# Kernel optimization log

Hardware: AMD Instinct MI355X
Metric: run time of the kernel (lower is better)

Reference implementation:

```python
import jax, jax.numpy as jnp
import numpy as np

N_NODES = 100000
N_EDGES = 3200000
F_IN = 512
F_OUT = 256


def setup_inputs() -> dict:
    key = jax.random.key(0)
    k1, k2, k3, k4, k5 = jax.random.split(key, 5)
    x = jax.random.normal(k1, (N_NODES, F_IN), dtype=jnp.float32)
    weights = jax.random.normal(k2, (F_IN, F_OUT), dtype=jnp.float32) * 0.05
    # sparse adjacency in COO, row-sorted (equivalent to the CSR torch.spmm uses)
    edge_row = jnp.sort(jax.random.randint(k3, (N_EDGES,), 0, N_NODES, dtype=jnp.int32))
    edge_col = jax.random.randint(k4, (N_EDGES,), 0, N_NODES, dtype=jnp.int32)
    edge_val = jax.random.uniform(k5, (N_EDGES,), dtype=jnp.float32)
    return {"x": x, "weights": weights, "edge_row": edge_row,
            "edge_col": edge_col, "edge_val": edge_val}


def reference(x, weights, edge_row, edge_col, edge_val):
    # support = input @ weights  (dense GEMM)
    support = jnp.matmul(x, weights)                      # [N, F_OUT]
    # output = spmm(adj, support): gather neighbor rows, scale, scatter-add
    gathered = support[edge_col] * edge_val[:, None]      # [E, F_OUT]
    out = jax.ops.segment_sum(gathered, edge_row, num_segments=N_NODES)
    return out
```

## Files before the change

### kernel.cpp

```cpp
#include <hip/hip_runtime.h>

#define N_NODES 100000
#define N_EDGES 3200000
#define F_IN 512
#define F_OUT 256

typedef short bf16x8 __attribute__((ext_vector_type(8)));
typedef float f32x4 __attribute__((ext_vector_type(4)));
typedef unsigned u32x4 __attribute__((ext_vector_type(4)));

__device__ __forceinline__ short f2b(float f) {
    unsigned u = __builtin_bit_cast(unsigned, f);
    u += 0x7fffu + ((u >> 16) & 1u);
    return (short)(u >> 16);
}
__device__ __forceinline__ float b2f(short s) {
    unsigned u = ((unsigned)(unsigned short)s) << 16;
    return __builtin_bit_cast(float, u);
}
__device__ __forceinline__ unsigned pack2(float f0, float f1) {
    unsigned u0 = __builtin_bit_cast(unsigned, f0) + 0x8000u;
    unsigned u1 = __builtin_bit_cast(unsigned, f1) + 0x8000u;
    return __builtin_amdgcn_perm(u1, u0, 0x07060302);
}
__device__ __forceinline__ void load_lds16(const float* g, void* l) {
    __builtin_amdgcn_global_load_lds(
        (const __attribute__((address_space(1))) unsigned*)g,
        (__attribute__((address_space(3))) unsigned*)l, 16, 0, 0);
}

__global__ void k_wconv(const float* __restrict__ W, short* __restrict__ Wt) {
    int idx = blockIdx.x * 256 + threadIdx.x;
    int k = idx >> 8;
    int n = idx & 255;
    Wt[n * F_IN + k] = f2b(W[idx]);
}

__global__ void k_rowptr(const int* __restrict__ erow, int* __restrict__ rp) {
    int i = blockIdx.x * 256 + threadIdx.x;
    if (i > N_NODES) return;
    int lo = 0, hi = N_EDGES;
    while (lo < hi) {
        int mid = (lo + hi) >> 1;
        if (erow[mid] < i) lo = mid + 1; else hi = mid;
    }
    rp[i] = lo;
}

__global__ __launch_bounds__(512, 4) void k_gemm(const float* __restrict__ X,
                                                 const short* __restrict__ Wt,
                                                 short* __restrict__ S) {
    __shared__ float As[2][128 * 32];
    const int tid  = threadIdx.x;
    const int wave = tid >> 6;
    const int lane = tid & 63;
    const int wr   = wave >> 2;
    const int wc   = wave & 3;
    const int l15  = lane & 15, quad = lane >> 4;
    const long row_base = (long)blockIdx.x * 128;

    f32x4 acc[4][4];
#pragma unroll
    for (int i = 0; i < 4; ++i)
#pragma unroll
        for (int j = 0; j < 4; ++j) acc[i][j] = (f32x4){0.f, 0.f, 0.f, 0.f};

    const int srow = tid >> 3;
    const int schunk = (tid & 7) ^ (srow & 7);
    long gr0 = row_base + srow;
    long gr1 = gr0 + 64;
    if (gr0 >= N_NODES) gr0 = N_NODES - 1;
    if (gr1 >= N_NODES) gr1 = N_NODES - 1;
    const float* gp0 = X + gr0 * F_IN + schunk * 4;
    const float* gp1 = X + gr1 * F_IN + schunk * 4;
    char* lbase = (char*)As + wave * 1024;

    const short* wtb = Wt + (wc * 64 + l15) * F_IN + quad * 8;
    const int sw = l15 & 7;
    const int c0 = ((quad * 2) ^ sw) * 16;
    const int c1 = ((quad * 2 + 1) ^ sw) * 16;
    const int arow_byte = (wr * 64 + l15) * 128;

    bf16x8 bcur[4];
#pragma unroll
    for (int j = 0; j < 4; ++j)
        bcur[j] = *(const bf16x8*)(wtb + j * 16 * F_IN);
    load_lds16(gp0, lbase);
    load_lds16(gp1, lbase + 8192);

#pragma unroll 1
    for (int k0 = 0; k0 < F_IN; k0 += 32) {
        const int cur = (k0 >> 5) & 1;
        bf16x8 bnxt[4];
        if (k0 + 32 < F_IN) {
#pragma unroll
            for (int j = 0; j < 4; ++j)
                bnxt[j] = *(const bf16x8*)(wtb + j * 16 * F_IN + k0 + 32);
            char* lnext = lbase + (cur ^ 1) * 16384;
            load_lds16(gp0 + k0 + 32, lnext);
            load_lds16(gp1 + k0 + 32, lnext + 8192);
            asm volatile("s_waitcnt vmcnt(6)" ::: "memory");
        } else {
            asm volatile("s_waitcnt vmcnt(0)" ::: "memory");
        }
        __builtin_amdgcn_s_barrier();

        const char* abase = (const char*)As + cur * 16384 + arow_byte;
#pragma unroll
        for (int i = 0; i < 4; ++i) {
            const char* ap = abase + i * 16 * 128;
            f32x4 x0 = *(const f32x4*)(ap + c0);
            f32x4 x1 = *(const f32x4*)(ap + c1);
            u32x4 pv = { pack2(x0.x, x0.y), pack2(x0.z, x0.w),
                         pack2(x1.x, x1.y), pack2(x1.z, x1.w) };
            bf16x8 afrag = __builtin_bit_cast(bf16x8, pv);
#pragma unroll
            for (int j = 0; j < 4; ++j)
                acc[i][j] = __builtin_amdgcn_mfma_f32_16x16x32_bf16(
                    afrag, bcur[j], acc[i][j], 0, 0, 0);
        }

        asm volatile("s_waitcnt lgkmcnt(0)" ::: "memory");
        __builtin_amdgcn_s_barrier();
        if (k0 + 32 < F_IN) {
#pragma unroll
            for (int j = 0; j < 4; ++j) bcur[j] = bnxt[j];
        }
    }

#pragma unroll
    for (int i = 0; i < 4; ++i) {
#pragma unroll
        for (int rg = 0; rg < 4; ++rg) {
            long gm = row_base + wr * 64 + i * 16 + quad * 4 + rg;
            if (gm < N_NODES) {
#pragma unroll
                for (int j = 0; j < 4; ++j) {
                    int gn = wc * 64 + j * 16 + l15;
                    S[gm * F_OUT + gn] = f2b(acc[i][j][rg]);
                }
            }
        }
    }
}

__global__ __launch_bounds__(256) void k_spmm(const short* __restrict__ S,
                                              const int* __restrict__ ecol,
                                              const float* __restrict__ ev,
                                              const int* __restrict__ rp,
                                              float* __restrict__ out) {
    const int wave = threadIdx.x >> 6, lane = threadIdx.x & 63;
    const int half = lane >> 5, hl = lane & 31;
    const int r = (blockIdx.x * 4 + wave) * 2 + half;
    const int lo = rp[r], hi = rp[r + 1];
    const short* sp = S + hl * 8;
    const int lb = half * 32;
    float a[8] = {0.f, 0.f, 0.f, 0.f, 0.f, 0.f, 0.f, 0.f};

#pragma unroll 1
    for (int base = lo; base < hi; base += 32) {
        int eidx = base + hl;
        bool inb = eidx < hi;
        int   cl = inb ? ecol[eidx] : 0;
        float vl = inb ? ev[eidx]   : 0.f;
        int n = hi - base; if (n > 32) n = 32;
        int n4 = (n + 3) & ~3;

        float vc[4]; bf16x8 ss[4];
#pragma unroll
        for (int u = 0; u < 4; ++u) {
            int c = __shfl(cl, lb + u);
            vc[u] = __shfl(vl, lb + u);
            ss[u] = *(const bf16x8*)(sp + c * 256);
        }
#pragma unroll 1
        for (int j = 4; j < n4; j += 4) {
            float nv[4]; bf16x8 ns[4];
#pragma unroll
            for (int u = 0; u < 4; ++u) {
                int c = __shfl(cl, lb + j + u);
                nv[u] = __shfl(vl, lb + j + u);
                ns[u] = *(const bf16x8*)(sp + c * 256);
            }
#pragma unroll
            for (int u = 0; u < 4; ++u)
#pragma unroll
                for (int i = 0; i < 8; ++i)
                    a[i] += vc[u] * b2f(ss[u][i]);
#pragma unroll
            for (int u = 0; u < 4; ++u) { vc[u] = nv[u]; ss[u] = ns[u]; }
        }
#pragma unroll
        for (int u = 0; u < 4; ++u)
#pragma unroll
            for (int i = 0; i < 8; ++i)
                a[i] += vc[u] * b2f(ss[u][i]);
    }
    f32x4 o0 = {a[0], a[1], a[2], a[3]};
    f32x4 o1 = {a[4], a[5], a[6], a[7]};
    float* op = out + (long)r * F_OUT + hl * 8;
    *(f32x4*)op = o0;
    *(f32x4*)(op + 4) = o1;
}

extern "C" void kernel_launch(void* const* d_in, const int* in_sizes, int n_in,
                              void* d_out, int out_size, void* d_ws, size_t ws_size,
                              hipStream_t stream) {
    const float* x    = (const float*)d_in[0];
    const float* w    = (const float*)d_in[1];
    const int*   erow = (const int*)d_in[2];
    const int*   ecol = (const int*)d_in[3];
    const float* ev   = (const float*)d_in[4];
    float* out = (float*)d_out;

    char* ws = (char*)d_ws;
    short* Wt = (short*)ws;
    int*   rp = (int*)(ws + 262144);
    short* S  = (short*)(ws + (1 << 20));

    k_wconv<<<512, 256, 0, stream>>>(w, Wt);
    k_rowptr<<<(N_NODES + 256) / 256, 256, 0, stream>>>(erow, rp);
    k_gemm<<<(N_NODES + 127) / 128, 512, 0, stream>>>(x, Wt, S);
    k_spmm<<<N_NODES / 8, 256, 0, stream>>>(S, ecol, ev, rp, out);
}
```

Measured before the change: 606.4 us.

## Stage GEMM weight tiles through LDS and use one wave per row in SpMM

The GEMM now brings the bf16 weight tile into a swizzled, double-buffered LDS region with global_load_lds, instead of each wave reading its B fragments straight from global memory into registers. This means blocks share the weight traffic, at the cost of doubling LDS use to 64KB, which may lower occupancy. The SpMM kernel changes from two rows per wave with shuffles to one row per wave. Edge indices and values are read as scalars via readfirstlane, each lane gathers 4 bf16 values, and eight gathers are issued per batch to raise memory-level parallelism.

```diff
diff --git a/kernel.cpp b/kernel.cpp
--- a/kernel.cpp
+++ b/kernel.cpp
@@ -6,6 +6,7 @@
 #define F_OUT 256
 
 typedef short bf16x8 __attribute__((ext_vector_type(8)));
+typedef short bf16x4 __attribute__((ext_vector_type(4)));
 typedef float f32x4 __attribute__((ext_vector_type(4)));
 typedef unsigned u32x4 __attribute__((ext_vector_type(4)));
 
@@ -23,7 +24,7 @@
     unsigned u1 = __builtin_bit_cast(unsigned, f1) + 0x8000u;
     return __builtin_amdgcn_perm(u1, u0, 0x07060302);
 }
-__device__ __forceinline__ void load_lds16(const float* g, void* l) {
+__device__ __forceinline__ void load_lds16(const void* g, void* l) {
     __builtin_amdgcn_global_load_lds(
         (const __attribute__((address_space(1))) unsigned*)g,
         (__attribute__((address_space(3))) unsigned*)l, 16, 0, 0);
@@ -50,7 +51,9 @@
 __global__ __launch_bounds__(512, 4) void k_gemm(const float* __restrict__ X,
                                                  const short* __restrict__ Wt,
                                                  short* __restrict__ S) {
-    __shared__ float As[2][128 * 32];
+    __shared__ char lds[65536];
+    char* ldsA = lds;
+    char* ldsB = lds + 32768;
     const int tid  = threadIdx.x;
     const int wave = tid >> 6;
     const int lane = tid & 63;
@@ -73,39 +76,53 @@
     if (gr1 >= N_NODES) gr1 = N_NODES - 1;
     const float* gp0 = X + gr0 * F_IN + schunk * 4;
     const float* gp1 = X + gr1 * F_IN + schunk * 4;
-    char* lbase = (char*)As + wave * 1024;
-
-    const short* wtb = Wt + (wc * 64 + l15) * F_IN + quad * 8;
+
+    const int bidx0 = wave * 128 + lane;
+    const int bn0 = bidx0 >> 2, bs0 = bidx0 & 3;
+    const int bidx1 = bidx0 + 64;
+    const int bn1 = bidx1 >> 2, bs1 = bidx1 & 3;
+    const short* bsrc0 = Wt + bn0 * F_IN + (bs0 ^ (bn0 & 3)) * 8;
+    const short* bsrc1 = Wt + bn1 * F_IN + (bs1 ^ (bn1 & 3)) * 8;
+
     const int sw = l15 & 7;
     const int c0 = ((quad * 2) ^ sw) * 16;
     const int c1 = ((quad * 2 + 1) ^ sw) * 16;
     const int arow_byte = (wr * 64 + l15) * 128;
-
-    bf16x8 bcur[4];
-#pragma unroll
-    for (int j = 0; j < 4; ++j)
-        bcur[j] = *(const bf16x8*)(wtb + j * 16 * F_IN);
-    load_lds16(gp0, lbase);
-    load_lds16(gp1, lbase + 8192);
+    const int bchunk = (quad ^ (l15 & 3)) * 16;
+    const int brow_byte = (wc * 64 + l15) * 64;
+
+    {
+        char* a0 = ldsA + wave * 1024;
+        load_lds16(gp0, a0);
+        load_lds16(gp1, a0 + 8192);
+        char* b0 = ldsB + wave * 2048;
+        load_lds16(bsrc0, b0);
+        load_lds16(bsrc1, b0 + 1024);
+    }
 
 #pragma unroll 1
     for (int k0 = 0; k0 < F_IN; k0 += 32) {
         const int cur = (k0 >> 5) & 1;
-        bf16x8 bnxt[4];
         if (k0 + 32 < F_IN) {
-#pragma unroll
-            for (int j = 0; j < 4; ++j)
-                bnxt[j] = *(const bf16x8*)(wtb + j * 16 * F_IN + k0 + 32);
-            char* lnext = lbase + (cur ^ 1) * 16384;
-            load_lds16(gp0 + k0 + 32, lnext);
-            load_lds16(gp1 + k0 + 32, lnext + 8192);
-            asm volatile("s_waitcnt vmcnt(6)" ::: "memory");
+            const int kk = k0 + 32;
+            char* a0 = ldsA + (cur ^ 1) * 16384 + wave * 1024;
+            load_lds16(gp0 + kk, a0);
+            load_lds16(gp1 + kk, a0 + 8192);
+            char* b0 = ldsB + (cur ^ 1) * 16384 + wave * 2048;
+            load_lds16(bsrc0 + kk, b0);
+            load_lds16(bsrc1 + kk, b0 + 1024);
+            asm volatile("s_waitcnt vmcnt(4)" ::: "memory");
         } else {
             asm volatile("s_waitcnt vmcnt(0)" ::: "memory");
         }
         __builtin_amdgcn_s_barrier();
 
-        const char* abase = (const char*)As + cur * 16384 + arow_byte;
+        const char* abase = ldsA + cur * 16384 + arow_byte;
+        const char* bbase = ldsB + cur * 16384 + brow_byte;
+        bf16x8 bfrag[4];
+#pragma unroll
+        for (int j = 0; j < 4; ++j)
+            bfrag[j] = *(const bf16x8*)(bbase + j * 1024 + bchunk);
 #pragma unroll
         for (int i = 0; i < 4; ++i) {
             const char* ap = abase + i * 16 * 128;
@@ -117,15 +134,11 @@
 #pragma unroll
             for (int j = 0; j < 4; ++j)
                 acc[i][j] = __builtin_amdgcn_mfma_f32_16x16x32_bf16(
-                    afrag, bcur[j], acc[i][j], 0, 0, 0);
+                    afrag, bfrag[j], acc[i][j], 0, 0, 0);
         }
 
         asm volatile("s_waitcnt lgkmcnt(0)" ::: "memory");
         __builtin_amdgcn_s_barrier();
-        if (k0 + 32 < F_IN) {
-#pragma unroll
-            for (int j = 0; j < 4; ++j) bcur[j] = bnxt[j];
-        }
     }
 
 #pragma unroll
@@ -149,58 +162,39 @@
                                               const float* __restrict__ ev,
                                               const int* __restrict__ rp,
                                               float* __restrict__ out) {
-    const int wave = threadIdx.x >> 6, lane = threadIdx.x & 63;
-    const int half = lane >> 5, hl = lane & 31;
-    const int r = (blockIdx.x * 4 + wave) * 2 + half;
-    const int lo = rp[r], hi = rp[r + 1];
-    const short* sp = S + hl * 8;
-    const int lb = half * 32;
-    float a[8] = {0.f, 0.f, 0.f, 0.f, 0.f, 0.f, 0.f, 0.f};
+    const int wid  = __builtin_amdgcn_readfirstlane((int)(threadIdx.x >> 6));
+    const int lane = threadIdx.x & 63;
+    const int r = blockIdx.x * 4 + wid;
+    const int lo = __builtin_amdgcn_readfirstlane(rp[r]);
+    const int hi = __builtin_amdgcn_readfirstlane(rp[r + 1]);
+    const short* sp = S + lane * 4;
+    float a0 = 0.f, a1 = 0.f, a2 = 0.f, a3 = 0.f;
 
 #pragma unroll 1
-    for (int base = lo; base < hi; base += 32) {
-        int eidx = base + hl;
-        bool inb = eidx < hi;
-        int   cl = inb ? ecol[eidx] : 0;
-        float vl = inb ? ev[eidx]   : 0.f;
-        int n = hi - base; if (n > 32) n = 32;
-        int n4 = (n + 3) & ~3;
-
-        float vc[4]; bf16x8 ss[4];
-#pragma unroll
-        for (int u = 0; u < 4; ++u) {
-            int c = __shfl(cl, lb + u);
-            vc[u] = __shfl(vl, lb + u);
-            ss[u] = *(const bf16x8*)(sp + c * 256);
-        }
-#pragma unroll 1
-        for (int j = 4; j < n4; j += 4) {
-            float nv[4]; bf16x8 ns[4];
-#pragma unroll
-            for (int u = 0; u < 4; ++u) {
-                int c = __shfl(cl, lb + j + u);
-                nv[u] = __shfl(vl, lb + j + u);
-                ns[u] = *(const bf16x8*)(sp + c * 256);
-            }
-#pragma unroll
-            for (int u = 0; u < 4; ++u)
-#pragma unroll
-                for (int i = 0; i < 8; ++i)
-                    a[i] += vc[u] * b2f(ss[u][i]);
-#pragma unroll
-            for (int u = 0; u < 4; ++u) { vc[u] = nv[u]; ss[u] = ns[u]; }
-        }
-#pragma unroll
-        for (int u = 0; u < 4; ++u)
-#pragma unroll
-            for (int i = 0; i < 8; ++i)
-                a[i] += vc[u] * b2f(ss[u][i]);
-    }
-    f32x4 o0 = {a[0], a[1], a[2], a[3]};
-    f32x4 o1 = {a[4], a[5], a[6], a[7]};
-    float* op = out + (long)r * F_OUT + hl * 8;
-    *(f32x4*)op = o0;
-    *(f32x4*)(op + 4) = o1;
+    for (int base = lo; base < hi; base += 8) {
+        int cc[8]; float vv[8];
+#pragma unroll
+        for (int u = 0; u < 8; ++u) {
+            int e = base + u;
+            int ee = e < hi ? e : hi - 1;
+            cc[u] = __builtin_amdgcn_readfirstlane(ecol[ee]);
+            int vb = __builtin_bit_cast(int, e < hi ? ev[ee] : 0.f);
+            vv[u] = __builtin_bit_cast(float, __builtin_amdgcn_readfirstlane(vb));
+        }
+        bf16x4 g[8];
+#pragma unroll
+        for (int u = 0; u < 8; ++u)
+            g[u] = *(const bf16x4*)(sp + cc[u] * 256);
+#pragma unroll
+        for (int u = 0; u < 8; ++u) {
+            a0 += vv[u] * b2f(g[u][0]);
+            a1 += vv[u] * b2f(g[u][1]);
+            a2 += vv[u] * b2f(g[u][2]);
+            a3 += vv[u] * b2f(g[u][3]);
+        }
+    }
+    f32x4 o = {a0, a1, a2, a3};
+    *(f32x4*)(out + (long)r * F_OUT + lane * 4) = o;
 }
 
 extern "C" void kernel_launch(void* const* d_in, const int* in_sizes, int n_in,
@@ -221,5 +215,5 @@
     k_wconv<<<512, 256, 0, stream>>>(w, Wt);
     k_rowptr<<<(N_NODES + 256) / 256, 256, 0, stream>>>(erow, rp);
     k_gemm<<<(N_NODES + 127) / 128, 512, 0, stream>>>(x, Wt, S);
-    k_spmm<<<N_NODES / 8, 256, 0, stream>>>(S, ecol, ev, rp, out);
-}
+    k_spmm<<<N_NODES / 4, 256, 0, stream>>>(S, ecol, ev, rp, out);
+}
```

Result: faster. 579.1 us (-4.5%).
